# Kernel optimization log

Hardware: AMD Instinct MI355X
Metric: run time of the kernel (lower is better)

## Reference

```python
import jax, jax.numpy as jnp
import numpy as np

B, N, F_IN, F_OUT = 64, 4096, 32, 32


def setup_inputs() -> dict:
    key = jax.random.key(0)
    k1, k2, k3, k4 = jax.random.split(key, 4)
    x = jax.random.normal(k1, (B, N, F_IN), dtype=jnp.float32)
    adj = jax.random.uniform(k2, (N, N), dtype=jnp.float32)
    # GraphConvolution parameters (Glorot-ish scale)
    W = jax.random.normal(k3, (F_IN, F_OUT), dtype=jnp.float32) / np.sqrt(F_IN)
    b = jax.random.normal(k4, (F_OUT,), dtype=jnp.float32) * 0.01
    return {"x": x, "adj": adj, "W": W, "b": b}


def reference(x, adj, W, b):
    # Original: adj_ = kron(I_B, adj) -> block-diagonal [B*N, B*N];
    # gconv(x_flat, adj_) = adj_ @ (x_flat @ W) + b, reshaped to [B, N, F_OUT].
    # Block-diagonal structure == independent per-batch graph conv:
    #   out[b] = adj @ (x[b] @ W) + b
    support = jnp.einsum('bnf,fo->bno', x, W)      # [B, N, F_OUT]
    out = jnp.einsum('nm,bmo->bno', adj, support)  # [B, N, F_OUT]
    return out + b
```

## Files before the change

kernel.cpp:

```cpp
#include <hip/hip_runtime.h>
#include <hip/hip_bf16.h>


#define B_SZ 64
#define N_SZ 4096
#define NT 64

typedef __attribute__((ext_vector_type(8))) short bf16x8;
typedef __attribute__((ext_vector_type(4))) float f32x4;
typedef __attribute__((ext_vector_type(8))) unsigned short u16x8;

__device__ __forceinline__ unsigned short f2bf(float f) {
  unsigned int u = __float_as_uint(f);
  u += 0x7fffu + ((u >> 16) & 1u);
  return (unsigned short)(u >> 16);
}

__device__ __forceinline__ void support_body_lds(const float* __restrict__ x,
                                                 const float* __restrict__ W,
                                                 unsigned short* __restrict__ St,
                                                 int sbid, int t,
                                                 unsigned short* __restrict__ L) {
  const int b = sbid >> 4;
  const int m0 = (sbid & 15) << 8;
  const int gid = (sbid << 8) + t;
  const float4* xr = (const float4*)(x + (size_t)gid * 32);
  float xv[32];
#pragma unroll
  for (int i = 0; i < 8; ++i) {
    float4 v = xr[i];
    xv[4 * i + 0] = v.x; xv[4 * i + 1] = v.y;
    xv[4 * i + 2] = v.z; xv[4 * i + 3] = v.w;
  }
#pragma unroll
  for (int o = 0; o < 32; ++o) {
    float acc = 0.f;
#pragma unroll
    for (int f = 0; f < 32; ++f) acc = fmaf(xv[f], W[f * 32 + o], acc);
    L[t * 33 + o] = f2bf(acc);
  }
  __syncthreads();
  const int l32 = t & 31;
#pragma unroll
  for (int it = 0; it < 4; ++it) {
    const int o = it * 8 + (t >> 5);
    u16x8 w;
#pragma unroll
    for (int i = 0; i < 8; ++i) w[i] = L[(l32 * 8 + i) * 33 + o];
    *(u16x8*)(St + ((size_t)(b * 32 + o) << 12) + m0 + l32 * 8) = w;
  }
}

__device__ __forceinline__ void cvt_body(const float* __restrict__ a,
                                         unsigned short* __restrict__ o,
                                         size_t idx8) {
  const size_t i = idx8 * 8;
  const float4* p = (const float4*)(a + i);
  float4 v0 = p[0], v1 = p[1];
  u16x8 r;
  r[0] = f2bf(v0.x); r[1] = f2bf(v0.y); r[2] = f2bf(v0.z); r[3] = f2bf(v0.w);
  r[4] = f2bf(v1.x); r[5] = f2bf(v1.y); r[6] = f2bf(v1.z); r[7] = f2bf(v1.w);
  *(u16x8*)(o + i) = r;
}

__global__ __launch_bounds__(256) void k_prep(const float* __restrict__ x,
                                              const float* __restrict__ adj,
                                              const float* __restrict__ W,
                                              unsigned short* __restrict__ St,
                                              unsigned short* __restrict__ adjB) {
  __shared__ unsigned short L[256 * 33];
  const int bid = blockIdx.x;
  const int t = threadIdx.x;
  if (bid < 8192) cvt_body(adj, adjB, (size_t)bid * 256 + t);
  else support_body_lds(x, W, St, bid - 8192, t, L);
}

__global__ __launch_bounds__(256) void k_support(const float* __restrict__ x,
                                                 const float* __restrict__ W,
                                                 unsigned short* __restrict__ St) {
  __shared__ unsigned short L[256 * 33];
  support_body_lds(x, W, St, blockIdx.x, threadIdx.x, L);
}
__global__ __launch_bounds__(256) void k_cvt(const float* __restrict__ a,
                                             unsigned short* __restrict__ o) {
  cvt_body(a, o, (size_t)blockIdx.x * 256 + threadIdx.x);
}

#define GLOAD16(gp, lp)                                                        \
  __builtin_amdgcn_global_load_lds(                                            \
      (const __attribute__((address_space(1))) void*)(gp),                     \
      (__attribute__((address_space(3))) void*)(lp), 16, 0, 0)
#define PRIO1() __builtin_amdgcn_s_setprio(1)
#define PRIO0() __builtin_amdgcn_s_setprio(0)

__global__ __launch_bounds__(256, 2) void k_gemm6(const unsigned short* __restrict__ Ab,
                                                  const unsigned short* __restrict__ Bm,
                                                  const float* __restrict__ bias,
                                                  float* __restrict__ out,
                                                  int nbm, int rowoff) {
  __shared__ __attribute__((aligned(16))) char SM[65536];
  char* Lc = SM;
  char* Lo = SM + 32768;
  const int t = threadIdx.x;
  const int wg = blockIdx.x;
  const int xcd = wg & 7;
  const int idx = wg >> 3;
  int bm0, bn0;
  if (nbm == 4) {
    bm0 = ((xcd >> 1) << 10) + ((idx >> 3) << 7);
    bn0 = ((xcd & 1) << 10) + ((idx & 7) << 7);
  } else {
    bm0 = (xcd * nbm + (idx >> 4)) << 7;
    bn0 = (idx & 15) << 7;
  }
  const int lane = t & 63;
  const int wid = t >> 6;
  const int wr = wid & 1;
  const int ks = wid >> 1;

  f32x4 acc[4][8];
#pragma unroll
  for (int i = 0; i < 4; ++i)
#pragma unroll
    for (int j = 0; j < 8; ++j) acc[i][j] = (f32x4){0.f, 0.f, 0.f, 0.f};

  const int srow = t >> 3;
  const int as = t & 7;
  const int swz = (as ^ (srow & 7)) << 4;
  const size_t a_s0 = ((size_t)(bm0 + srow) << 13) + (size_t)swz;
  const size_t b_s0 = ((size_t)(bn0 + srow) << 13) + (size_t)swz;
  const int t16 = t * 16;
  const char* A8 = (const char*)Ab;
  const char* B8 = (const char*)Bm;

#define STAGE(KT_, Ld)                                                         \
  do {                                                                         \
    const size_t kb = (size_t)(KT_) << 7;                                      \
    GLOAD16(A8 + a_s0 + kb,          (Ld) + t16);                              \
    GLOAD16(A8 + a_s0 + 262144 + kb, (Ld) + 4096 + t16);                       \
    GLOAD16(A8 + a_s0 + 524288 + kb, (Ld) + 8192 + t16);                       \
    GLOAD16(A8 + a_s0 + 786432 + kb, (Ld) + 12288 + t16);                      \
    GLOAD16(B8 + b_s0 + kb,          (Ld) + 16384 + t16);                      \
    GLOAD16(B8 + b_s0 + 262144 + kb, (Ld) + 20480 + t16);                      \
    GLOAD16(B8 + b_s0 + 524288 + kb, (Ld) + 24576 + t16);                      \
    GLOAD16(B8 + b_s0 + 786432 + kb, (Ld) + 28672 + t16);                      \
  } while (0)

  const int cbase = (ks * 64 + ((lane >> 4) << 4)) ^ ((lane & 7) << 4);
  int aoff[4], boff[8];
#pragma unroll
  for (int mi = 0; mi < 4; ++mi)
    aoff[mi] = (wr * 64 + mi * 16 + (lane & 15)) * 128 + cbase;
#pragma unroll
  for (int ni = 0; ni < 8; ++ni)
    boff[ni] = 16384 + (ni * 16 + (lane & 15)) * 128 + cbase;

  STAGE(0, Lc);
  __syncthreads();

  for (int kt = 0; kt < NT; ++kt) {
    if (kt + 1 < NT) STAGE(kt + 1, Lo);
    bf16x8 a[4], b[8];
#pragma unroll
    for (int mi = 0; mi < 4; ++mi) a[mi] = *(const bf16x8*)(Lc + aoff[mi]);
#pragma unroll
    for (int ni = 0; ni < 8; ++ni) b[ni] = *(const bf16x8*)(Lc + boff[ni]);
    PRIO1();
#pragma unroll
    for (int mi = 0; mi < 4; ++mi)
#pragma unroll
      for (int ni = 0; ni < 8; ++ni)
        acc[mi][ni] = __builtin_amdgcn_mfma_f32_16x16x32_bf16(
            a[mi], b[ni], acc[mi][ni], 0, 0, 0);
    PRIO0();
    __syncthreads();
    { char* tp_ = Lc; Lc = Lo; Lo = tp_; }
  }

  if (ks == 1) {
    char* mb = SM + (wr << 15);
#pragma unroll
    for (int mi = 0; mi < 4; ++mi)
#pragma unroll
      for (int ni = 0; ni < 8; ++ni)
        *(f32x4*)(mb + (((mi * 8 + ni) << 6) + lane) * 16) = acc[mi][ni];
  }
  __syncthreads();
  if (ks == 0) {
    char* mb = SM + (wr << 15);
#pragma unroll
    for (int mi = 0; mi < 4; ++mi)
#pragma unroll
      for (int ni = 0; ni < 8; ++ni)
        acc[mi][ni] += *(const f32x4*)(mb + (((mi * 8 + ni) << 6) + lane) * 16);
    const float blo = bias[lane & 15];
    const float bhi = bias[(lane & 15) + 16];
#pragma unroll
    for (int mi = 0; mi < 4; ++mi) {
#pragma unroll
      for (int ni = 0; ni < 8; ++ni) {
        const float badd = (ni & 1) ? bhi : blo;
#pragma unroll
        for (int q = 0; q < 4; ++q) {
          const int n = rowoff + bm0 + wr * 64 + mi * 16 + ((lane >> 4) << 2) + q;
          const int cidx = bn0 + ni * 16 + (lane & 15);
          const int bb = cidx >> 5;
          const int o = cidx & 31;
          out[(((size_t)bb << 12) + n) * 32 + o] = acc[mi][ni][q] + badd;
        }
      }
    }
  }
}

extern "C" void kernel_launch(void* const* d_in, const int* in_sizes, int n_in,
                              void* d_out, int out_size, void* d_ws, size_t ws_size,
                              hipStream_t stream) {
  const float* x = (const float*)d_in[0];
  const float* adj = (const float*)d_in[1];
  const float* W = (const float*)d_in[2];
  const float* bias = (const float*)d_in[3];
  float* out = (float*)d_out;

  const size_t ST_B = (size_t)2048 * 4096 * 2;
  const size_t ADJ_FULL = (size_t)4096 * 4096 * 2;

  unsigned short* St = (unsigned short*)d_ws;

  if (ws_size >= ST_B + ADJ_FULL) {
    unsigned short* adjB = St + (ST_B / 2);
    hipLaunchKernelGGL(k_prep, dim3(9216), dim3(256), 0, stream, x, adj, W, St,
                       adjB);
    hipLaunchKernelGGL(k_gemm6, dim3(512), dim3(256), 0, stream, adjB, St, bias,
                       out, 4, 0);
  } else {
    unsigned short* adjH = St + (ST_B / 2);
    hipLaunchKernelGGL(k_support, dim3((B_SZ * N_SZ) / 256), dim3(256), 0,
                       stream, x, W, St);
    hipLaunchKernelGGL(k_cvt, dim3((2048 * 4096) / 2048), dim3(256), 0, stream,
                       adj, adjH);
    hipLaunchKernelGGL(k_gemm6, dim3(256), dim3(256), 0, stream, adjH, St, bias,
                       out, 2, 0);
    hipLaunchKernelGGL(k_cvt, dim3((2048 * 4096) / 2048), dim3(256), 0, stream,
                       adj + (size_t)2048 * 4096, adjH);
    hipLaunchKernelGGL(k_gemm6, dim3(256), dim3(256), 0, stream, adjH, St, bias,
                       out, 2, 2048);
  }
}
```

Measured before the change: 90.11 us.

## Compute support projection with split-bf16 MFMA and schedule support blocks first

Replaces the per-thread scalar FMA loop for x@W with bf16 MFMA instructions. Both x and W are split into hi/lo bf16 parts and three MFMAs are accumulated to keep near-fp32 accuracy. Inputs are staged in XOR-swizzled LDS to avoid bank conflicts. The prep kernel also reorders blocks so the support blocks are dispatched before the adj conversion blocks, and it uses a larger 36 KB LDS buffer, which may reduce occupancy for the conversion blocks.

Result: faster. 84.74 us (-6.0%).

```diff
diff --git a/kernel.cpp b/kernel.cpp
--- a/kernel.cpp
+++ b/kernel.cpp
@@ -15,30 +15,96 @@
   u += 0x7fffu + ((u >> 16) & 1u);
   return (unsigned short)(u >> 16);
 }
-
-__device__ __forceinline__ void support_body_lds(const float* __restrict__ x,
-                                                 const float* __restrict__ W,
-                                                 unsigned short* __restrict__ St,
-                                                 int sbid, int t,
-                                                 unsigned short* __restrict__ L) {
+__device__ __forceinline__ float bf2f(unsigned short h) {
+  return __uint_as_float(((unsigned int)h) << 16);
+}
+
+__device__ __forceinline__ void support_mfma(const float* __restrict__ x,
+                                             const float* __restrict__ W,
+                                             unsigned short* __restrict__ St,
+                                             int sbid, int t, char* SB) {
+  unsigned short* Ah = (unsigned short*)SB;
+  unsigned short* Al = (unsigned short*)(SB + 16384);
+  unsigned short* Wh = (unsigned short*)(SB + 32768);
+  unsigned short* Wl = (unsigned short*)(SB + 34816);
   const int b = sbid >> 4;
   const int m0 = (sbid & 15) << 8;
-  const int gid = (sbid << 8) + t;
-  const float4* xr = (const float4*)(x + (size_t)gid * 32);
-  float xv[32];
-#pragma unroll
-  for (int i = 0; i < 8; ++i) {
-    float4 v = xr[i];
-    xv[4 * i + 0] = v.x; xv[4 * i + 1] = v.y;
-    xv[4 * i + 2] = v.z; xv[4 * i + 3] = v.w;
-  }
-#pragma unroll
-  for (int o = 0; o < 32; ++o) {
-    float acc = 0.f;
-#pragma unroll
-    for (int f = 0; f < 32; ++f) acc = fmaf(xv[f], W[f * 32 + o], acc);
-    L[t * 33 + o] = f2bf(acc);
-  }
+  const float* xb = x + ((size_t)sbid << 13);
+#pragma unroll
+  for (int j = 0; j < 4; ++j) {
+    const int idx8 = t + 256 * j;
+    const int node = idx8 >> 2;
+    const int ch = idx8 & 3;
+    const float4* xp = (const float4*)(xb + (size_t)idx8 * 8);
+    float4 v0 = xp[0], v1 = xp[1];
+    float vv[8] = {v0.x, v0.y, v0.z, v0.w, v1.x, v1.y, v1.z, v1.w};
+    u16x8 hi, lo;
+#pragma unroll
+    for (int i = 0; i < 8; ++i) {
+      unsigned short h = f2bf(vv[i]);
+      hi[i] = h;
+      lo[i] = f2bf(vv[i] - bf2f(h));
+    }
+    const int aoffb = node * 64 + ((ch ^ (node & 3)) << 4);
+    *(u16x8*)((char*)Ah + aoffb) = hi;
+    *(u16x8*)((char*)Al + aoffb) = lo;
+  }
+#pragma unroll
+  for (int i = 0; i < 4; ++i) {
+    const int e = t * 4 + i;
+    const int o = e >> 5;
+    const int f = e & 31;
+    const float wv = W[f * 32 + o];
+    const unsigned short wh = f2bf(wv);
+    const unsigned short wl = f2bf(wv - bf2f(wh));
+    const int wb = o * 64 + ((((f >> 3) ^ (o & 3)) << 4)) + (f & 7) * 2;
+    *(unsigned short*)((char*)Wh + wb) = wh;
+    *(unsigned short*)((char*)Wl + wb) = wl;
+  }
+  __syncthreads();
+  const int lane = t & 63;
+  const int wid = t >> 6;
+  const int kch = lane >> 4;
+  bf16x8 ah[4], al[4], bh[2], bl[2];
+#pragma unroll
+  for (int mi = 0; mi < 4; ++mi) {
+    const int row = wid * 64 + mi * 16 + (lane & 15);
+    const int off = row * 64 + ((kch ^ (row & 3)) << 4);
+    ah[mi] = *(const bf16x8*)((char*)Ah + off);
+    al[mi] = *(const bf16x8*)((char*)Al + off);
+  }
+#pragma unroll
+  for (int nj = 0; nj < 2; ++nj) {
+    const int o = nj * 16 + (lane & 15);
+    const int off = o * 64 + ((kch ^ (o & 3)) << 4);
+    bh[nj] = *(const bf16x8*)((char*)Wh + off);
+    bl[nj] = *(const bf16x8*)((char*)Wl + off);
+  }
+  f32x4 acc[4][2];
+#pragma unroll
+  for (int mi = 0; mi < 4; ++mi)
+#pragma unroll
+    for (int nj = 0; nj < 2; ++nj) {
+      acc[mi][nj] = (f32x4){0.f, 0.f, 0.f, 0.f};
+      acc[mi][nj] = __builtin_amdgcn_mfma_f32_16x16x32_bf16(ah[mi], bl[nj],
+                                                            acc[mi][nj], 0, 0, 0);
+      acc[mi][nj] = __builtin_amdgcn_mfma_f32_16x16x32_bf16(al[mi], bh[nj],
+                                                            acc[mi][nj], 0, 0, 0);
+      acc[mi][nj] = __builtin_amdgcn_mfma_f32_16x16x32_bf16(ah[mi], bh[nj],
+                                                            acc[mi][nj], 0, 0, 0);
+    }
+  __syncthreads();
+  unsigned short* L = (unsigned short*)SB;
+#pragma unroll
+  for (int mi = 0; mi < 4; ++mi)
+#pragma unroll
+    for (int nj = 0; nj < 2; ++nj)
+#pragma unroll
+      for (int q = 0; q < 4; ++q) {
+        const int nl = wid * 64 + mi * 16 + ((lane >> 4) << 2) + q;
+        const int o = nj * 16 + (lane & 15);
+        L[nl * 33 + o] = f2bf(acc[mi][nj][q]);
+      }
   __syncthreads();
   const int l32 = t & 31;
 #pragma unroll
@@ -68,18 +134,18 @@
                                               const float* __restrict__ W,
                                               unsigned short* __restrict__ St,
                                               unsigned short* __restrict__ adjB) {
-  __shared__ unsigned short L[256 * 33];
+  __shared__ __attribute__((aligned(16))) char SB[36864];
   const int bid = blockIdx.x;
   const int t = threadIdx.x;
-  if (bid < 8192) cvt_body(adj, adjB, (size_t)bid * 256 + t);
-  else support_body_lds(x, W, St, bid - 8192, t, L);
+  if (bid < 1024) support_mfma(x, W, St, bid, t, SB);
+  else cvt_body(adj, adjB, (size_t)(bid - 1024) * 256 + t);
 }
 
 __global__ __launch_bounds__(256) void k_support(const float* __restrict__ x,
                                                  const float* __restrict__ W,
                                                  unsigned short* __restrict__ St) {
-  __shared__ unsigned short L[256 * 33];
-  support_body_lds(x, W, St, blockIdx.x, threadIdx.x, L);
+  __shared__ __attribute__((aligned(16))) char SB[36864];
+  support_mfma(x, W, St, blockIdx.x, threadIdx.x, SB);
 }
 __global__ __launch_bounds__(256) void k_cvt(const float* __restrict__ a,
                                              unsigned short* __restrict__ o) {
```
